# Optimization experiments

Measured on AMD Instinct MI355X. Metric: run time of the kernel, lower is better.

Reference implementation:

```python
import jax, jax.numpy as jnp
import numpy as np

FIELD_DIMS = [50000] * 24
NUM_FIELDS = len(FIELD_DIMS)
EMBED_DIM = 16
ATTN_SIZE = 32
TOTAL_VOCAB = int(np.sum(FIELD_DIMS))
OFFSETS = jnp.asarray(np.concatenate([[0], np.cumsum(FIELD_DIMS)[:-1]]), dtype=jnp.int64)
# all unordered field pairs (i < j)
_ROWS, _COLS = np.triu_indices(NUM_FIELDS, k=1)
ROWS = jnp.asarray(_ROWS)
COLS = jnp.asarray(_COLS)


def setup_inputs() -> dict:
    key = jax.random.key(0)
    ks = jax.random.split(key, 9)
    B = 16384
    x = jax.random.randint(ks[0], (B, NUM_FIELDS), 0, 50000, dtype=jnp.int64)
    s = 0.05
    return {
        "x": x,
        "embed_table": jax.random.normal(ks[1], (TOTAL_VOCAB, EMBED_DIM), jnp.float32) * s,
        "linear_table": jax.random.normal(ks[2], (TOTAL_VOCAB, 1), jnp.float32) * s,
        "linear_bias": jnp.zeros((1,), jnp.float32),
        "attn_W": jax.random.normal(ks[3], (EMBED_DIM, ATTN_SIZE), jnp.float32) * s,
        "attn_b": jnp.zeros((ATTN_SIZE,), jnp.float32),
        "proj_w": jax.random.normal(ks[4], (ATTN_SIZE, 1), jnp.float32) * s,
        "proj_b": jnp.zeros((1,), jnp.float32),
        "fc_w": jax.random.normal(ks[5], (EMBED_DIM, 1), jnp.float32) * s,
        "fc_b": jnp.zeros((1,), jnp.float32),
    }


def reference(x, embed_table, linear_table, linear_bias, attn_W, attn_b, proj_w, proj_b, fc_w, fc_b):
    idx = x + OFFSETS[None, :]                      # [B, F] global row ids
    emb = embed_table[idx]                          # [B, F, E]
    linear_term = linear_table[idx].sum(axis=1) + linear_bias  # [B, 1]
    # pairwise elementwise products
    inner = emb[:, ROWS, :] * emb[:, COLS, :]       # [B, P, E]
    # attention MLP over pairs
    h = jax.nn.relu(jnp.einsum('bpe,ea->bpa', inner, attn_W) + attn_b)  # [B, P, A]
    scores = jnp.einsum('bpa,ao->bpo', h, proj_w) + proj_b              # [B, P, 1]
    attn = jax.nn.softmax(scores, axis=1)           # softmax over pairs
    pooled = jnp.sum(attn * inner, axis=1)          # [B, E]
    cross_term = pooled @ fc_w + fc_b               # [B, 1]
    return linear_term + cross_term
```

## Files before the change

kernel.cpp:

```cpp
#include <hip/hip_runtime.h>
#include <hip/hip_bf16.h>
#include <float.h>


#define FN 24
#define ED 16
#define AS 32
#define NP 276
#define NT 9
#define LASTV 20
#define EPITCH 20
#define RPW 4
#define NTHR 256
#define FIELD_SIZE 50000

typedef __attribute__((ext_vector_type(8)))  short bf16x8;
typedef __attribute__((ext_vector_type(16))) float f32x16;
typedef __attribute__((ext_vector_type(2)))  float f32x2;

union BFR { int i[4]; bf16x8 v; };

__device__ __forceinline__ short f2bf(float x) {
    union { __hip_bfloat16 h; short s; } u;
    u.h = __float2bfloat16(x);
    return u.s;
}

__device__ __forceinline__ void gather_embed(const float* __restrict__ et,
                                             int idxv, int lane,
                                             float4& a, float4& b) {
    const int f0 = lane >> 2, q0 = lane & 3;
    const int id0 = __shfl(idxv, f0, 64);
    const int id1 = __shfl(idxv, 16 + f0, 64);
    a = ((const float4*)(et + (size_t)id0 * ED))[q0];
    if (lane < 32)
        b = ((const float4*)(et + (size_t)id1 * ED))[q0];
}

__device__ __forceinline__ void write_embed(float* __restrict__ buf, int lane,
                                            const float4& a, const float4& b) {
    const int f0 = lane >> 2, q0 = lane & 3;
    *(float4*)&buf[f0 * EPITCH + q0 * 4] = a;
    if (lane < 32)
        *(float4*)&buf[(16 + f0) * EPITCH + q0 * 4] = b;
}

__global__ __launch_bounds__(NTHR, 4) void afm_kernel(
    const int*   __restrict__ x,
    const float* __restrict__ embed_table,
    const float* __restrict__ linear_table,
    const float* __restrict__ linear_bias,
    const float* __restrict__ attn_W,
    const float* __restrict__ attn_b,
    const float* __restrict__ proj_w,
    const float* __restrict__ fc_w,
    const float* __restrict__ fc_b,
    float*       __restrict__ out,
    int B)
{
    __shared__ float emb_s[NTHR / 64][2][FN * EPITCH];
    __shared__ int   pko_s[NT * 32];

    const int tid  = threadIdx.x;
    const int wave = tid >> 6;
    const int lane = tid & 63;
    const int half = lane >> 5;
    const int col  = lane & 31;
    const int e0   = half * 8;
    const int w0   = (blockIdx.x * (NTHR / 64) + wave) * RPW;

    for (int s = tid; s < NT * 32; s += NTHR) {
        const int p = (s < NP) ? s : (NP - 1);
        const int q = (NP - 1) - p;
        int m = (int)((sqrtf((float)(8 * q + 1)) + 1.0f) * 0.5f);
        if (m * (m + 1) / 2 <= q) ++m;
        if ((m - 1) * m / 2 > q) --m;
        const int fi = (FN - 1) - m;
        const int fj = fi + 1 + (p - (NP - m * (m + 1) / 2));
        pko_s[s] = ((fi * (EPITCH * 4)) << 16) | (fj * (EPITCH * 4));
    }

    int idxr[RPW];
#pragma unroll
    for (int k = 0; k < RPW; ++k) {
        const int r = w0 + k, rc = (r < B) ? r : (B - 1);
        idxr[k] = (lane < FN) ? (x[rc * FN + lane] + lane * FIELD_SIZE) : 0;
    }

    bf16x8 aW;
#pragma unroll
    for (int i = 0; i < 8; ++i) aW[i] = f2bf(attn_W[(e0 + i) * AS + col]);
    float b16[16], pw16[16];
#pragma unroll
    for (int r = 0; r < 16; ++r) {
        const int a = (r & 3) + 8 * (r >> 2) + 4 * half;
        b16[r]  = attn_b[a];
        pw16[r] = proj_w[a];
    }
    float fcw[8];
#pragma unroll
    for (int i = 0; i < 8; ++i) fcw[i] = fc_w[e0 + i];
    const float cbias = linear_bias[0] + fc_b[0];

    float linv = (lane < FN) ? linear_table[idxr[0]] : 0.f;
    {
        float4 ga, gb;
        gather_embed(embed_table, idxr[0], lane, ga, gb);
        write_embed(emb_s[wave][0], lane, ga, gb);
    }

    __syncthreads();
    int pk[NT];
#pragma unroll
    for (int t = 0; t < NT; ++t) pk[t] = pko_s[t * 32 + col];

#pragma unroll
    for (int k = 0; k < RPW; ++k) {
        const int row = w0 + k;
        float4 na, nb; float linn = 0.f;
        if (k + 1 < RPW) {
            linn = (lane < FN) ? linear_table[idxr[k + 1]] : 0.f;
            gather_embed(embed_table, idxr[k + 1], lane, na, nb);
        }

        const char* embb = (const char*)emb_s[wave][k & 1] + half * 32;
        float m = -FLT_MAX, ssum = 0.f, gacc = 0.f;
#pragma unroll
        for (int t = 0; t < NT; ++t) {
            const int oi = pk[t] >> 16;
            const int oj = pk[t] & 0xffff;
            const float4 xi0 = *(const float4*)(embb + oi);
            const float4 xi1 = *(const float4*)(embb + oi + 16);
            const float4 xj0 = *(const float4*)(embb + oj);
            const float4 xj1 = *(const float4*)(embb + oj + 16);
            const float p0 = xi0.x * xj0.x, p1 = xi0.y * xj0.y;
            const float p2 = xi0.z * xj0.z, p3 = xi0.w * xj0.w;
            const float p4 = xi1.x * xj1.x, p5 = xi1.y * xj1.y;
            const float p6 = xi1.z * xj1.z, p7 = xi1.w * xj1.w;
            float gv = p0 * fcw[0];
            gv = fmaf(p1, fcw[1], gv); gv = fmaf(p2, fcw[2], gv);
            gv = fmaf(p3, fcw[3], gv); gv = fmaf(p4, fcw[4], gv);
            gv = fmaf(p5, fcw[5], gv); gv = fmaf(p6, fcw[6], gv);
            gv = fmaf(p7, fcw[7], gv);
            BFR u;
            u.i[0] = __builtin_amdgcn_perm(__float_as_int(p1), __float_as_int(p0), 0x07060302);
            u.i[1] = __builtin_amdgcn_perm(__float_as_int(p3), __float_as_int(p2), 0x07060302);
            u.i[2] = __builtin_amdgcn_perm(__float_as_int(p5), __float_as_int(p4), 0x07060302);
            u.i[3] = __builtin_amdgcn_perm(__float_as_int(p7), __float_as_int(p6), 0x07060302);
            f32x16 c;
#pragma unroll
            for (int r = 0; r < 16; ++r) c[r] = b16[r];
            c = __builtin_amdgcn_mfma_f32_32x32x16_bf16(aW, u.v, c, 0, 0, 0);
            f32x2 sac; sac.x = 0.f; sac.y = 0.f;
            f32x2 z2;  z2.x = 0.f;  z2.y = 0.f;
#pragma unroll
            for (int r2 = 0; r2 < 8; ++r2) {
                f32x2 h; h.x = c[2 * r2]; h.y = c[2 * r2 + 1];
                h = __builtin_elementwise_max(h, z2);
                f32x2 pw; pw.x = pw16[2 * r2]; pw.y = pw16[2 * r2 + 1];
                sac = __builtin_elementwise_fma(h, pw, sac);
            }
            float s = sac.x + sac.y;
            s += __shfl_xor(s, 32, 64);
            const bool valid = (t < NT - 1) || (col < LASTV);
            s = valid ? s : -FLT_MAX;
            const float mn   = fmaxf(m, s);
            const float cold = __expf(m - mn);
            const float e    = __expf(s - mn);
            ssum = fmaf(ssum, cold, e);
            gacc = fmaf(gacc, cold, e * gv);
            m = mn;
        }

        float M = m;
#pragma unroll
        for (int off = 16; off; off >>= 1) M = fmaxf(M, __shfl_xor(M, off, 64));
        const float rs = __expf(m - M);
        ssum *= rs; gacc *= rs;
#pragma unroll
        for (int off = 16; off; off >>= 1) ssum += __shfl_xor(ssum, off, 64);
#pragma unroll
        for (int off = 32; off; off >>= 1) gacc += __shfl_xor(gacc, off, 64);
        float lin = linv;
#pragma unroll
        for (int off = 32; off; off >>= 1) lin += __shfl_xor(lin, off, 64);

        if (row < B && lane == 0)
            out[row] = lin + cbias + gacc / ssum;

        if (k + 1 < RPW) {
            write_embed(emb_s[wave][(k + 1) & 1], lane, na, nb);
            linv = linn;
        }
    }
}

extern "C" void kernel_launch(void* const* d_in, const int* in_sizes, int n_in,
                              void* d_out, int out_size, void* d_ws, size_t ws_size,
                              hipStream_t stream) {
    const int*   x            = (const int*)  d_in[0];
    const float* embed_table  = (const float*)d_in[1];
    const float* linear_table = (const float*)d_in[2];
    const float* linear_bias  = (const float*)d_in[3];
    const float* attn_W       = (const float*)d_in[4];
    const float* attn_b       = (const float*)d_in[5];
    const float* proj_w       = (const float*)d_in[6];
    const float* fc_w         = (const float*)d_in[8];
    const float* fc_b         = (const float*)d_in[9];
    float* out = (float*)d_out;

    const int B = in_sizes[0] / FN;
    const int rows_per_block = (NTHR / 64) * RPW;
    const int grid = (B + rows_per_block - 1) / rows_per_block;
    afm_kernel<<<grid, NTHR, 0, stream>>>(x, embed_table, linear_table,
                                          linear_bias, attn_W, attn_b, proj_w,
                                          fc_w, fc_b, out, B);
}
```

Before: 140.7 us.

## Prefetch next pair's LDS operands, vectorize products, and shrink rows per wave

Reduces rows per wave from 4 to 2, which doubles the grid size, and lowers the launch-bounds occupancy hint from 4 to 3 blocks. Inside the pair loop it double-buffers the LDS loads, fetching the next tile's embedding vectors while the current tile's MFMA runs. It also rewrites the pair products and the fc dot product as 4-wide vector ops and splits the ReLU/projection accumulation into two independent chains to shorten dependencies. The changes aim to hide LDS latency and add parallelism, at the cost of more registers and more blocks that each amortize the setup over fewer rows.

Result: slower. 145.2 us (+3.1%).

```diff
diff --git a/kernel.cpp b/kernel.cpp
--- a/kernel.cpp
+++ b/kernel.cpp
@@ -10,12 +10,13 @@
 #define NT 9
 #define LASTV 20
 #define EPITCH 20
-#define RPW 4
+#define RPW 2
 #define NTHR 256
 #define FIELD_SIZE 50000
 
 typedef __attribute__((ext_vector_type(8)))  short bf16x8;
 typedef __attribute__((ext_vector_type(16))) float f32x16;
+typedef __attribute__((ext_vector_type(4)))  float f32x4v;
 typedef __attribute__((ext_vector_type(2)))  float f32x2;
 
 union BFR { int i[4]; bf16x8 v; };
@@ -45,7 +46,7 @@
         *(float4*)&buf[(16 + f0) * EPITCH + q0 * 4] = b;
 }
 
-__global__ __launch_bounds__(NTHR, 4) void afm_kernel(
+__global__ __launch_bounds__(NTHR, 3) void afm_kernel(
     const int*   __restrict__ x,
     const float* __restrict__ embed_table,
     const float* __restrict__ linear_table,
@@ -90,16 +91,21 @@
     bf16x8 aW;
 #pragma unroll
     for (int i = 0; i < 8; ++i) aW[i] = f2bf(attn_W[(e0 + i) * AS + col]);
-    float b16[16], pw16[16];
+    float b16[16];
+    f32x2 pw2_[8];
 #pragma unroll
     for (int r = 0; r < 16; ++r) {
         const int a = (r & 3) + 8 * (r >> 2) + 4 * half;
-        b16[r]  = attn_b[a];
-        pw16[r] = proj_w[a];
-    }
-    float fcw[8];
-#pragma unroll
-    for (int i = 0; i < 8; ++i) fcw[i] = fc_w[e0 + i];
+        b16[r] = attn_b[a];
+        if (r & 1) pw2_[r >> 1].y = proj_w[a];
+        else       pw2_[r >> 1].x = proj_w[a];
+    }
+    f32x4v fcwA, fcwB;
+#pragma unroll
+    for (int i = 0; i < 4; ++i) {
+        fcwA[i] = fc_w[e0 + i];
+        fcwB[i] = fc_w[e0 + 4 + i];
+    }
     const float cbias = linear_bias[0] + fc_b[0];
 
     float linv = (lane < FN) ? linear_table[idxr[0]] : 0.f;
@@ -124,43 +130,52 @@
         }
 
         const char* embb = (const char*)emb_s[wave][k & 1] + half * 32;
+
+        f32x4v xi0[2], xi1[2], xj0[2], xj1[2];
+        {
+            const int oi = pk[0] >> 16, oj = pk[0] & 0xffff;
+            xi0[0] = *(const f32x4v*)(embb + oi);
+            xi1[0] = *(const f32x4v*)(embb + oi + 16);
+            xj0[0] = *(const f32x4v*)(embb + oj);
+            xj1[0] = *(const f32x4v*)(embb + oj + 16);
+        }
+
         float m = -FLT_MAX, ssum = 0.f, gacc = 0.f;
 #pragma unroll
         for (int t = 0; t < NT; ++t) {
-            const int oi = pk[t] >> 16;
-            const int oj = pk[t] & 0xffff;
-            const float4 xi0 = *(const float4*)(embb + oi);
-            const float4 xi1 = *(const float4*)(embb + oi + 16);
-            const float4 xj0 = *(const float4*)(embb + oj);
-            const float4 xj1 = *(const float4*)(embb + oj + 16);
-            const float p0 = xi0.x * xj0.x, p1 = xi0.y * xj0.y;
-            const float p2 = xi0.z * xj0.z, p3 = xi0.w * xj0.w;
-            const float p4 = xi1.x * xj1.x, p5 = xi1.y * xj1.y;
-            const float p6 = xi1.z * xj1.z, p7 = xi1.w * xj1.w;
-            float gv = p0 * fcw[0];
-            gv = fmaf(p1, fcw[1], gv); gv = fmaf(p2, fcw[2], gv);
-            gv = fmaf(p3, fcw[3], gv); gv = fmaf(p4, fcw[4], gv);
-            gv = fmaf(p5, fcw[5], gv); gv = fmaf(p6, fcw[6], gv);
-            gv = fmaf(p7, fcw[7], gv);
+            const int cur = t & 1, nxt = cur ^ 1;
+            if (t + 1 < NT) {
+                const int oi = pk[t + 1] >> 16, oj = pk[t + 1] & 0xffff;
+                xi0[nxt] = *(const f32x4v*)(embb + oi);
+                xi1[nxt] = *(const f32x4v*)(embb + oi + 16);
+                xj0[nxt] = *(const f32x4v*)(embb + oj);
+                xj1[nxt] = *(const f32x4v*)(embb + oj + 16);
+            }
+            const f32x4v pa = xi0[cur] * xj0[cur];
+            const f32x4v pb = xi1[cur] * xj1[cur];
+            f32x4v g4 = __builtin_elementwise_fma(pb, fcwB, pa * fcwA);
+            const float gv = (g4.x + g4.y) + (g4.z + g4.w);
             BFR u;
-            u.i[0] = __builtin_amdgcn_perm(__float_as_int(p1), __float_as_int(p0), 0x07060302);
-            u.i[1] = __builtin_amdgcn_perm(__float_as_int(p3), __float_as_int(p2), 0x07060302);
-            u.i[2] = __builtin_amdgcn_perm(__float_as_int(p5), __float_as_int(p4), 0x07060302);
-            u.i[3] = __builtin_amdgcn_perm(__float_as_int(p7), __float_as_int(p6), 0x07060302);
+            u.i[0] = __builtin_amdgcn_perm(__float_as_int(pa.y), __float_as_int(pa.x), 0x07060302);
+            u.i[1] = __builtin_amdgcn_perm(__float_as_int(pa.w), __float_as_int(pa.z), 0x07060302);
+            u.i[2] = __builtin_amdgcn_perm(__float_as_int(pb.y), __float_as_int(pb.x), 0x07060302);
+            u.i[3] = __builtin_amdgcn_perm(__float_as_int(pb.w), __float_as_int(pb.z), 0x07060302);
             f32x16 c;
 #pragma unroll
             for (int r = 0; r < 16; ++r) c[r] = b16[r];
             c = __builtin_amdgcn_mfma_f32_32x32x16_bf16(aW, u.v, c, 0, 0, 0);
-            f32x2 sac; sac.x = 0.f; sac.y = 0.f;
-            f32x2 z2;  z2.x = 0.f;  z2.y = 0.f;
-#pragma unroll
-            for (int r2 = 0; r2 < 8; ++r2) {
-                f32x2 h; h.x = c[2 * r2]; h.y = c[2 * r2 + 1];
-                h = __builtin_elementwise_max(h, z2);
-                f32x2 pw; pw.x = pw16[2 * r2]; pw.y = pw16[2 * r2 + 1];
-                sac = __builtin_elementwise_fma(h, pw, sac);
+            const f32x2 z2 = {0.f, 0.f};
+            f32x2 sac0 = z2, sac1 = z2;
+#pragma unroll
+            for (int r2 = 0; r2 < 4; ++r2) {
+                f32x2 h0; h0.x = c[2 * r2]; h0.y = c[2 * r2 + 1];
+                h0 = __builtin_elementwise_max(h0, z2);
+                sac0 = __builtin_elementwise_fma(h0, pw2_[r2], sac0);
+                f32x2 h1; h1.x = c[8 + 2 * r2]; h1.y = c[8 + 2 * r2 + 1];
+                h1 = __builtin_elementwise_max(h1, z2);
+                sac1 = __builtin_elementwise_fma(h1, pw2_[4 + r2], sac1);
             }
-            float s = sac.x + sac.y;
+            float s = (sac0.x + sac0.y) + (sac1.x + sac1.y);
             s += __shfl_xor(s, 32, 64);
             const bool valid = (t < NT - 1) || (col < LASTV);
             s = valid ? s : -FLT_MAX;
```
